# Kernel optimization log

Measured on AMD Instinct MI355X. Metric: run time of the kernel, lower is better.

Reference implementation:

```python
import jax, jax.numpy as jnp
import numpy as np
from jax import lax


def _conv(x, w):
    # x: [B,H,W,C], w: [kh,kw,Cin,Cout], stride 1, 'same' padding
    return lax.conv_general_dilated(x, w, window_strides=(1, 1), padding='SAME',
                                    dimension_numbers=('NHWC', 'HWIO', 'NHWC'))


def setup_inputs() -> dict:
    key = jax.random.key(0)
    ks = jax.random.split(key, 4)
    B, T, H, W, Cin, F = 16, 5, 256, 256, 3, 8
    return {
        'input_tensor': jax.random.normal(ks[0], (B, T, H, W, Cin), jnp.float32),
        'kernel': jax.random.normal(ks[1], (3, 3, Cin, 4 * F), jnp.float32) * 0.1,
        'recurrent_kernel': jax.random.normal(ks[2], (3, 3, F, 4 * F), jnp.float32) * 0.1,
        'bias': jnp.zeros((4 * F,), jnp.float32),
        'gamma': jnp.ones((F,), jnp.float32),
        'beta': jnp.zeros((F,), jnp.float32),
        'moving_mean': jnp.zeros((F,), jnp.float32),
        'moving_var': jnp.ones((F,), jnp.float32),
        'dense_w': jax.random.normal(ks[3], (F, 2), jnp.float32) * 0.1,
        'dense_b': jnp.zeros((2,), jnp.float32),
    }


def reference(input_tensor, kernel, recurrent_kernel, bias, gamma, beta,
              moving_mean, moving_var, dense_w, dense_b):
    B, T, H, W, Cin = input_tensor.shape
    F = recurrent_kernel.shape[2]
    xs = jnp.moveaxis(input_tensor, 1, 0)  # [T,B,H,W,Cin] time-major for scan
    h0 = jnp.zeros((B, H, W, F), input_tensor.dtype)

    def step(carry, x_t):
        h, c = carry
        # fused 4-gate pre-activations, Keras gate order: i, f, c(g), o
        z = _conv(x_t, kernel) + _conv(h, recurrent_kernel) + bias
        i, f, g, o = jnp.split(z, 4, axis=-1)
        i = jax.nn.sigmoid(i)
        f = jax.nn.sigmoid(f)
        g = jnp.tanh(g)
        o = jax.nn.sigmoid(o)
        c = f * c + i * g
        h = o * jnp.tanh(c)
        return (h, c), None

    (h, _), _ = lax.scan(step, (h0, h0), xs)  # return_sequences=False -> last h

    # BatchNormalization (inference, Keras eps=1e-3)
    eps = 1e-3
    x = (h - moving_mean) * lax.rsqrt(moving_var + eps) * gamma + beta
    # LeakyReLU, Keras default alpha=0.3
    x = jnp.where(x >= 0, x, 0.3 * x)
    # Dense(2) over channel dim
    return jnp.einsum('bhwf,fk->bhwk', x, dense_w) + dense_b
```

## Files before the change

kernel.cpp:

```cpp
#include <hip/hip_runtime.h>


#define BB  16
#define TT  5
#define HH  256
#define WW  256
#define CIN 3
#define FF  8
#define GG  32

#define TWO 32
#define THO 32
#define RW  40
#define RH  40
#define LWW 42
#define LHH 42
#define NR  10

#define LOG2E 1.44269504088896340736f

typedef _Float16 half8  __attribute__((ext_vector_type(8)));
typedef _Float16 half4  __attribute__((ext_vector_type(4)));
typedef float    floatx4 __attribute__((ext_vector_type(4)));

__device__ __forceinline__ float frcp(float x) { return __builtin_amdgcn_rcpf(x); }
__device__ __forceinline__ float sig2(float z)  { return frcp(1.0f + __builtin_amdgcn_exp2f(z)); }
__device__ __forceinline__ float tanh2(float z) { return 1.0f - 2.0f * frcp(1.0f + __builtin_amdgcn_exp2f(z)); }

#define MFMA(A, B, C) __builtin_amdgcn_mfma_f32_16x16x32_f16((A), (B), (C), 0, 0, 0)

__global__ void build_frags(const float* __restrict__ wk,
                            const float* __restrict__ wr,
                            _Float16* __restrict__ blob) {
    const int lane = threadIdx.x & 63;
    const int quad = lane >> 4, nlo = lane & 15;
    for (int chunk = 0; chunk < 5; ++chunk) {
        for (int nh = 0; nh < 2; ++nh) {
            const int n = nh * 16 + nlo;
            const float scale = (n >= 16 && n < 24) ? (2.0f * LOG2E) : (-LOG2E);
            const int frag = chunk * 2 + nh;
            _Float16* dhi = blob + ((size_t)frag * 64 + lane) * 8;
            _Float16* dlo = (chunk >= 2)
                ? blob + ((size_t)(10 + (chunk - 2) * 2 + nh) * 64 + lane) * 8
                : nullptr;
            for (int j = 0; j < 8; ++j) {
                const int k = quad * 8 + j;
                float w = 0.0f;
                if (chunk == 0) {
                    int tap = k >> 2, ci = k & 3;
                    if (ci < 3) w = wk[(tap * 3 + ci) * GG + n];
                } else if (chunk == 1) {
                    if (quad == 0 && j < 3) w = wk[(8 * 3 + j) * GG + n];
                } else {
                    int c = chunk - 2;
                    int tap = c * 4 + quad, ci = j;
                    if (tap < 9) w = wr[(tap * FF + ci) * GG + n];
                }
                w *= scale;
                _Float16 wh = (_Float16)w;
                dhi[j] = wh;
                if (dlo) dlo[j] = (_Float16)(w - (float)wh);
            }
        }
    }
}

__global__ __launch_bounds__(256, 2) void lstm_fused(
    const float* __restrict__ xg,
    const _Float16* __restrict__ blob,
    const float* __restrict__ bias,
    const float* __restrict__ gamma, const float* __restrict__ beta,
    const float* __restrict__ mean,  const float* __restrict__ var,
    const float* __restrict__ dw,    const float* __restrict__ db,
    float* __restrict__ out)
{
    __shared__ half8 hAs[LHH * LWW];
    __shared__ half8 hBs[LHH * LWW];
    __shared__ half4 xls[LHH * LWW];

    const int tid  = threadIdx.x;
    const int bx = blockIdx.x, by = blockIdx.y, b = blockIdx.z;
    const int lane = tid & 63, wave = tid >> 6;
    const int quad = lane >> 4, nlo = lane & 15;
    const bool lo8 = (nlo < 8);
    const int fc = nlo & 7;

    const int xt0 = 2 * quad, xt1 = xt0 + 1;
    const int xoff0 = (xt0 / 3) * LWW + (xt0 % 3);
    const int xoff1 = (xt1 / 3) * LWW + (xt1 % 3);
    const int xoff2 = 2 * LWW + 2;
    int hoff[3];
#pragma unroll
    for (int c = 0; c < 3; ++c) {
        int tap = c * 4 + quad;
        if (tap > 8) tap = 8;
        hoff[c] = (tap / 3) * LWW + (tap % 3);
    }

    half8 bfh[10], bfl[6];
#pragma unroll
    for (int i = 0; i < 10; ++i)
        bfh[i] = *(const half8*)(blob + ((size_t)i * 64 + lane) * 8);
#pragma unroll
    for (int i = 0; i < 6; ++i)
        bfl[i] = *(const half8*)(blob + ((size_t)(10 + i) * 64 + lane) * 8);

    const float bv0 = bias[nlo] * (-LOG2E);
    const float bv1 = bias[16 + nlo] * (lo8 ? 2.0f * LOG2E : -LOG2E);

    const float bn_s = gamma[fc] * rsqrtf(var[fc] + 1e-3f);
    const float bn_b = beta[fc] - mean[fc] * bn_s;
    const float dw0 = dw[fc * 2 + 0], dw1 = dw[fc * 2 + 1];
    const float db0 = db[0], db1 = db[1];

    const half8 hz = {(_Float16)0, (_Float16)0, (_Float16)0, (_Float16)0,
                      (_Float16)0, (_Float16)0, (_Float16)0, (_Float16)0};
    for (int l = tid; l < LHH * LWW; l += 256) { hAs[l] = hz; hBs[l] = hz; }

    float c0r[NR][3], c1r[NR][3];
#pragma unroll
    for (int r = 0; r < NR; ++r)
#pragma unroll
        for (int s = 0; s < 3; ++s) { c0r[r][s] = 0.f; c1r[r][s] = 0.f; }

    for (int t = 0; t < TT; ++t) {
        half8* hRd = (t & 1) ? hAs : hBs;
        half8* hWr = (t & 1) ? hBs : hAs;

        for (int l = tid; l < LHH * LWW; l += 256) {
            int rr = l / LWW, rc = l - rr * LWW;
            int iy = by * THO + rr - 5;
            int ix = bx * TWO + rc - 5;
            half4 vh = {(_Float16)0, (_Float16)0, (_Float16)0, (_Float16)0};
            if ((unsigned)iy < HH && (unsigned)ix < WW) {
                const float* p = xg + (((size_t)(b * TT + t) * HH + iy) * WW + ix) * CIN;
                vh.x = (_Float16)p[0]; vh.y = (_Float16)p[1]; vh.z = (_Float16)p[2];
            }
            xls[l] = vh;
        }
        __syncthreads();

#pragma unroll 1
        for (int r10 = 0; r10 < NR; ++r10) {
            const int row = wave * NR + r10;
            const int rowbase = row * LWW + nlo;

            half4 xp[3], xq[3], xs_[3];
            half8 ah[3][3];
#pragma unroll
            for (int s = 0; s < 3; ++s) {
                const int base = rowbase + s * 12;
                xp[s]  = xls[base + xoff0];
                xq[s]  = xls[base + xoff1];
                xs_[s] = xls[base + xoff2];
                if (t > 0) {
#pragma unroll
                    for (int c = 0; c < 3; ++c)
                        ah[s][c] = hRd[base + hoff[c]];
                }
            }

#pragma unroll
            for (int s = 0; s < 3; ++s) {
                const int gx0 = s * 12;

                half8 a_xA = (half8){xp[s].x, xp[s].y, xp[s].z, xp[s].w,
                                     xq[s].x, xq[s].y, xq[s].z, xq[s].w};
                half8 a_xB = (half8){xs_[s].x, xs_[s].y, xs_[s].z, xs_[s].w,
                                     xs_[s].x, xs_[s].y, xs_[s].z, xs_[s].w};

                floatx4 acc0 = {bv0, bv0, bv0, bv0};
                floatx4 acc1 = {bv1, bv1, bv1, bv1};
                acc0 = MFMA(a_xA, bfh[0], acc0);  acc1 = MFMA(a_xA, bfh[1], acc1);
                acc0 = MFMA(a_xB, bfh[2], acc0);  acc1 = MFMA(a_xB, bfh[3], acc1);
                if (t > 0) {
#pragma unroll
                    for (int c = 0; c < 3; ++c) {
                        acc0 = MFMA(ah[s][c], bfh[4 + c * 2], acc0);
                        acc1 = MFMA(ah[s][c], bfh[5 + c * 2], acc1);
                        acc0 = MFMA(ah[s][c], bfl[c * 2 + 0], acc0);
                        acc1 = MFMA(ah[s][c], bfl[c * 2 + 1], acc1);
                    }
                }

                float s0 = lo8 ? acc0[2] : acc0[0]; float r0 = __shfl_xor(s0, 8, 64);
                float s1 = lo8 ? acc0[3] : acc0[1]; float r1 = __shfl_xor(s1, 8, 64);
                float s2 = lo8 ? acc1[2] : acc1[0]; float r2 = __shfl_xor(s2, 8, 64);
                float s3 = lo8 ? acc1[3] : acc1[1]; float r3 = __shfl_xor(s3, 8, 64);

                const float zi0 = lo8 ? acc0[0] : r0, zi1 = lo8 ? acc0[1] : r1;
                const float zf0 = lo8 ? r0 : acc0[2], zf1 = lo8 ? r1 : acc0[3];
                const float zg0 = lo8 ? acc1[0] : r2, zg1 = lo8 ? acc1[1] : r3;
                const float zo0 = lo8 ? r2 : acc1[2], zo1 = lo8 ? r3 : acc1[3];

                const float ii0 = sig2(zi0), ff0 = sig2(zf0), gg0 = tanh2(zg0), oo0 = sig2(zo0);
                const float cn0 = ff0 * c0r[r10][s] + ii0 * gg0;
                const float hn0 = oo0 * tanh2(cn0 * (2.0f * LOG2E));
                const float ii1 = sig2(zi1), ff1 = sig2(zf1), gg1 = tanh2(zg1), oo1 = sig2(zo1);
                const float cn1 = ff1 * c1r[r10][s] + ii1 * gg1;
                const float hn1 = oo1 * tanh2(cn1 * (2.0f * LOG2E));
                c0r[r10][s] = cn0; c1r[r10][s] = cn1;

                const int m0 = quad * 4 + (lo8 ? 0 : 2);
                const int iy  = by * THO + row - 4;
                const int ix0 = bx * TWO + gx0 + m0 - 4;
                if (t < TT - 1) {
                    const bool iny = (unsigned)iy < HH;
                    const int idx = (row + 1) * LWW + (gx0 + m0 + 1);
                    _Float16* hp = (_Float16*)hWr;
                    hp[idx * 8 + fc] =
                        (iny && (unsigned)ix0 < WW) ? (_Float16)hn0 : (_Float16)0;
                    hp[(idx + 1) * 8 + fc] =
                        (iny && (unsigned)(ix0 + 1) < WW) ? (_Float16)hn1 : (_Float16)0;
                } else {
                    float y0 = bn_s * hn0 + bn_b; y0 = (y0 >= 0.f) ? y0 : 0.3f * y0;
                    float y1 = bn_s * hn1 + bn_b; y1 = (y1 >= 0.f) ? y1 : 0.3f * y1;
                    float p00 = y0 * dw0, p01 = y0 * dw1;
                    float p10 = y1 * dw0, p11 = y1 * dw1;
#pragma unroll
                    for (int m = 1; m <= 4; m <<= 1) {
                        p00 += __shfl_xor(p00, m, 64);
                        p01 += __shfl_xor(p01, m, 64);
                        p10 += __shfl_xor(p10, m, 64);
                        p11 += __shfl_xor(p11, m, 64);
                    }
                    const int j = nlo & 7;
                    if (j < 4) {
                        const int rc = gx0 + m0 + (j >> 1);
                        const int k  = j & 1;
                        if (rc >= 4 && rc < 36 && row >= 4 && row < 36) {
                            const int ox = bx * TWO + rc - 4;
                            const int oy = by * THO + row - 4;
                            float val = (j == 0 ? p00 : j == 1 ? p01 : j == 2 ? p10 : p11)
                                        + (k ? db1 : db0);
                            out[((size_t)(b * HH + oy) * WW + ox) * 2 + k] = val;
                        }
                    }
                }
            }
        }
        __syncthreads();
    }
}

extern "C" void kernel_launch(void* const* d_in, const int* in_sizes, int n_in,
                              void* d_out, int out_size, void* d_ws, size_t ws_size,
                              hipStream_t stream) {
    const float* x     = (const float*)d_in[0];
    const float* wk    = (const float*)d_in[1];
    const float* wr    = (const float*)d_in[2];
    const float* bias  = (const float*)d_in[3];
    const float* gamma = (const float*)d_in[4];
    const float* beta  = (const float*)d_in[5];
    const float* mean  = (const float*)d_in[6];
    const float* var   = (const float*)d_in[7];
    const float* dw    = (const float*)d_in[8];
    const float* db    = (const float*)d_in[9];
    float* out = (float*)d_out;

    _Float16* blob = (_Float16*)d_ws;

    build_frags<<<1, 64, 0, stream>>>(wk, wr, blob);

    dim3 grid(WW / TWO, HH / THO, BB);
    dim3 block(256);
    lstm_fused<<<grid, block, 0, stream>>>(
        x, blob, bias, gamma, beta, mean, var, dw, db, out);
}
```

Measured before the change: 304.3 us.

## Split time loop into three launches with global h/c state and smaller halos

Replaces the single fused kernel, which recomputed a 4-pixel halo per tile across all 5 timesteps, with three templated launches covering steps 0-1, 2-3 and 4. Between launches h and c are stored to global memory in fp16. This shrinks the halo to 2 pixels and the LDS tiles (34x22), cutting redundant halo compute and allowing more resident blocks. The cost is extra global traffic for the h/c state and launch overhead, and storing c in fp16 loses some precision.

```diff
diff --git a/kernel.cpp b/kernel.cpp
--- a/kernel.cpp
+++ b/kernel.cpp
@@ -9,13 +9,14 @@
 #define FF  8
 #define GG  32
 
-#define TWO 32
-#define THO 32
-#define RW  40
-#define RH  40
-#define LWW 42
-#define LHH 42
-#define NR  10
+#define TWO 28
+#define THO 16
+#define RW  32
+#define RH  20
+#define LWW 34
+#define LHH 22
+#define NRW 5
+#define GX  10
 
 #define LOG2E 1.44269504088896340736f
 
@@ -65,10 +66,15 @@
     }
 }
 
-__global__ __launch_bounds__(256, 2) void lstm_fused(
+template <int T0, int NS, bool FIRST, bool LAST>
+__global__ __launch_bounds__(256) void lstm_multi(
     const float* __restrict__ xg,
     const _Float16* __restrict__ blob,
     const float* __restrict__ bias,
+    const _Float16* __restrict__ hin,
+    _Float16* __restrict__ hout,
+    const _Float16* __restrict__ cin,
+    _Float16* __restrict__ cout,
     const float* __restrict__ gamma, const float* __restrict__ beta,
     const float* __restrict__ mean,  const float* __restrict__ var,
     const float* __restrict__ dw,    const float* __restrict__ db,
@@ -84,6 +90,7 @@
     const int quad = lane >> 4, nlo = lane & 15;
     const bool lo8 = (nlo < 8);
     const int fc = nlo & 7;
+    const int m0 = quad * 4 + (lo8 ? 0 : 2);
 
     const int xt0 = 2 * quad, xt1 = xt0 + 1;
     const int xoff0 = (xt0 / 3) * LWW + (xt0 % 3);
@@ -108,78 +115,109 @@
     const float bv0 = bias[nlo] * (-LOG2E);
     const float bv1 = bias[16 + nlo] * (lo8 ? 2.0f * LOG2E : -LOG2E);
 
-    const float bn_s = gamma[fc] * rsqrtf(var[fc] + 1e-3f);
-    const float bn_b = beta[fc] - mean[fc] * bn_s;
-    const float dw0 = dw[fc * 2 + 0], dw1 = dw[fc * 2 + 1];
-    const float db0 = db[0], db1 = db[1];
+    float bn_s = 0.f, bn_b = 0.f, dw0 = 0.f, dw1 = 0.f, db0 = 0.f, db1 = 0.f;
+    if (LAST) {
+        bn_s = gamma[fc] * rsqrtf(var[fc] + 1e-3f);
+        bn_b = beta[fc] - mean[fc] * bn_s;
+        dw0 = dw[fc * 2 + 0]; dw1 = dw[fc * 2 + 1];
+        db0 = db[0]; db1 = db[1];
+    }
 
     const half8 hz = {(_Float16)0, (_Float16)0, (_Float16)0, (_Float16)0,
                       (_Float16)0, (_Float16)0, (_Float16)0, (_Float16)0};
     for (int l = tid; l < LHH * LWW; l += 256) { hAs[l] = hz; hBs[l] = hz; }
 
-    float c0r[NR][3], c1r[NR][3];
-#pragma unroll
-    for (int r = 0; r < NR; ++r)
-#pragma unroll
-        for (int s = 0; s < 3; ++s) { c0r[r][s] = 0.f; c1r[r][s] = 0.f; }
-
-    for (int t = 0; t < TT; ++t) {
-        half8* hRd = (t & 1) ? hAs : hBs;
-        half8* hWr = (t & 1) ? hBs : hAs;
-
+    float c0r[NRW][2], c1r[NRW][2];
+#pragma unroll
+    for (int r = 0; r < NRW; ++r) { c0r[r][0] = c0r[r][1] = 0.f;
+                                    c1r[r][0] = c1r[r][1] = 0.f; }
+    if (!FIRST) {
+#pragma unroll
+        for (int r = 0; r < NRW; ++r) {
+#pragma unroll
+            for (int st = 0; st < 2; ++st) {
+                const int row = wave * NRW + r;
+                const int iy  = by * THO + row - 2;
+                const int ix0 = bx * TWO + st * 16 + m0 - 2;
+                if ((unsigned)iy < HH) {
+                    const size_t base = ((size_t)(b * HH + iy) * WW) * FF + fc;
+                    if ((unsigned)ix0 < WW)
+                        c0r[r][st] = (float)cin[base + (size_t)ix0 * FF];
+                    if ((unsigned)(ix0 + 1) < WW)
+                        c1r[r][st] = (float)cin[base + (size_t)(ix0 + 1) * FF];
+                }
+            }
+        }
         for (int l = tid; l < LHH * LWW; l += 256) {
             int rr = l / LWW, rc = l - rr * LWW;
-            int iy = by * THO + rr - 5;
-            int ix = bx * TWO + rc - 5;
+            int iy = by * THO + rr - 3, ix = bx * TWO + rc - 3;
+            half8 v = hz;
+            if ((unsigned)iy < HH && (unsigned)ix < WW)
+                v = *(const half8*)(hin + ((size_t)(b * HH + iy) * WW + ix) * FF);
+            hAs[l] = v;
+        }
+    }
+
+#pragma unroll
+    for (int s = 0; s < NS; ++s) {
+        __syncthreads();
+
+        for (int l = tid; l < LHH * LWW; l += 256) {
+            int rr = l / LWW, rc = l - rr * LWW;
+            int iy = by * THO + rr - 3, ix = bx * TWO + rc - 3;
             half4 vh = {(_Float16)0, (_Float16)0, (_Float16)0, (_Float16)0};
             if ((unsigned)iy < HH && (unsigned)ix < WW) {
-                const float* p = xg + (((size_t)(b * TT + t) * HH + iy) * WW + ix) * CIN;
+                const float* p = xg + (((size_t)(b * TT + T0 + s) * HH + iy) * WW + ix) * CIN;
                 vh.x = (_Float16)p[0]; vh.y = (_Float16)p[1]; vh.z = (_Float16)p[2];
             }
             xls[l] = vh;
         }
         __syncthreads();
 
-#pragma unroll 1
-        for (int r10 = 0; r10 < NR; ++r10) {
-            const int row = wave * NR + r10;
+        const bool hconv = (s > 0) || !FIRST;
+        half8* hRd = (s & 1) ? hBs : hAs;
+        half8* hWr = (s & 1) ? hAs : hBs;
+
+#pragma unroll
+        for (int r = 0; r < NRW; ++r) {
+            const int row = wave * NRW + r;
             const int rowbase = row * LWW + nlo;
 
-            half4 xp[3], xq[3], xs_[3];
-            half8 ah[3][3];
-#pragma unroll
-            for (int s = 0; s < 3; ++s) {
-                const int base = rowbase + s * 12;
-                xp[s]  = xls[base + xoff0];
-                xq[s]  = xls[base + xoff1];
-                xs_[s] = xls[base + xoff2];
-                if (t > 0) {
+            half4 xp[2], xq[2], xs_[2];
+            half8 ah[2][3];
+#pragma unroll
+            for (int st = 0; st < 2; ++st) {
+                const int base = rowbase + st * 16;
+                xp[st]  = xls[base + xoff0];
+                xq[st]  = xls[base + xoff1];
+                xs_[st] = xls[base + xoff2];
+                if (hconv) {
 #pragma unroll
                     for (int c = 0; c < 3; ++c)
-                        ah[s][c] = hRd[base + hoff[c]];
-                }
-            }
-
-#pragma unroll
-            for (int s = 0; s < 3; ++s) {
-                const int gx0 = s * 12;
-
-                half8 a_xA = (half8){xp[s].x, xp[s].y, xp[s].z, xp[s].w,
-                                     xq[s].x, xq[s].y, xq[s].z, xq[s].w};
-                half8 a_xB = (half8){xs_[s].x, xs_[s].y, xs_[s].z, xs_[s].w,
-                                     xs_[s].x, xs_[s].y, xs_[s].z, xs_[s].w};
+                        ah[st][c] = hRd[base + hoff[c]];
+                }
+            }
+
+#pragma unroll
+            for (int st = 0; st < 2; ++st) {
+                const int gx0 = st * 16;
+
+                half8 a_xA = (half8){xp[st].x, xp[st].y, xp[st].z, xp[st].w,
+                                     xq[st].x, xq[st].y, xq[st].z, xq[st].w};
+                half8 a_xB = (half8){xs_[st].x, xs_[st].y, xs_[st].z, xs_[st].w,
+                                     xs_[st].x, xs_[st].y, xs_[st].z, xs_[st].w};
 
                 floatx4 acc0 = {bv0, bv0, bv0, bv0};
                 floatx4 acc1 = {bv1, bv1, bv1, bv1};
                 acc0 = MFMA(a_xA, bfh[0], acc0);  acc1 = MFMA(a_xA, bfh[1], acc1);
                 acc0 = MFMA(a_xB, bfh[2], acc0);  acc1 = MFMA(a_xB, bfh[3], acc1);
-                if (t > 0) {
+                if (hconv) {
 #pragma unroll
                     for (int c = 0; c < 3; ++c) {
-                        acc0 = MFMA(ah[s][c], bfh[4 + c * 2], acc0);
-                        acc1 = MFMA(ah[s][c], bfh[5 + c * 2], acc1);
-                        acc0 = MFMA(ah[s][c], bfl[c * 2 + 0], acc0);
-                        acc1 = MFMA(ah[s][c], bfl[c * 2 + 1], acc1);
+                        acc0 = MFMA(ah[st][c], bfh[4 + c * 2], acc0);
+                        acc1 = MFMA(ah[st][c], bfh[5 + c * 2], acc1);
+                        acc0 = MFMA(ah[st][c], bfl[c * 2 + 0], acc0);
+                        acc1 = MFMA(ah[st][c], bfl[c * 2 + 1], acc1);
                     }
                 }
 
@@ -194,24 +232,38 @@
                 const float zo0 = lo8 ? r2 : acc1[2], zo1 = lo8 ? r3 : acc1[3];
 
                 const float ii0 = sig2(zi0), ff0 = sig2(zf0), gg0 = tanh2(zg0), oo0 = sig2(zo0);
-                const float cn0 = ff0 * c0r[r10][s] + ii0 * gg0;
+                const float cn0 = ff0 * c0r[r][st] + ii0 * gg0;
                 const float hn0 = oo0 * tanh2(cn0 * (2.0f * LOG2E));
                 const float ii1 = sig2(zi1), ff1 = sig2(zf1), gg1 = tanh2(zg1), oo1 = sig2(zo1);
-                const float cn1 = ff1 * c1r[r10][s] + ii1 * gg1;
+                const float cn1 = ff1 * c1r[r][st] + ii1 * gg1;
                 const float hn1 = oo1 * tanh2(cn1 * (2.0f * LOG2E));
-                c0r[r10][s] = cn0; c1r[r10][s] = cn1;
-
-                const int m0 = quad * 4 + (lo8 ? 0 : 2);
-                const int iy  = by * THO + row - 4;
-                const int ix0 = bx * TWO + gx0 + m0 - 4;
-                if (t < TT - 1) {
+                c0r[r][st] = cn0; c1r[r][st] = cn1;
+
+                const int iy  = by * THO + row - 2;
+                const int pc0 = gx0 + m0;
+                const int ix0 = bx * TWO + pc0 - 2;
+
+                if (s < NS - 1) {
                     const bool iny = (unsigned)iy < HH;
-                    const int idx = (row + 1) * LWW + (gx0 + m0 + 1);
+                    const int idx = (row + 1) * LWW + (pc0 + 1);
                     _Float16* hp = (_Float16*)hWr;
                     hp[idx * 8 + fc] =
                         (iny && (unsigned)ix0 < WW) ? (_Float16)hn0 : (_Float16)0;
                     hp[(idx + 1) * 8 + fc] =
                         (iny && (unsigned)(ix0 + 1) < WW) ? (_Float16)hn1 : (_Float16)0;
+                } else if (!LAST) {
+                    const bool trow = (row >= 2 && row < 2 + THO);
+                    const bool t0ok = trow && pc0 >= 2 && pc0 < 2 + TWO && (unsigned)ix0 < WW;
+                    const bool t1ok = trow && pc0 + 1 >= 2 && pc0 + 1 < 2 + TWO &&
+                                      (unsigned)(ix0 + 1) < WW;
+                    if (t0ok) {
+                        const size_t p = ((size_t)(b * HH + iy) * WW + ix0) * FF + fc;
+                        hout[p] = (_Float16)hn0; cout[p] = (_Float16)cn0;
+                    }
+                    if (t1ok) {
+                        const size_t p = ((size_t)(b * HH + iy) * WW + ix0 + 1) * FF + fc;
+                        hout[p] = (_Float16)hn1; cout[p] = (_Float16)cn1;
+                    }
                 } else {
                     float y0 = bn_s * hn0 + bn_b; y0 = (y0 >= 0.f) ? y0 : 0.3f * y0;
                     float y1 = bn_s * hn1 + bn_b; y1 = (y1 >= 0.f) ? y1 : 0.3f * y1;
@@ -226,11 +278,12 @@
                     }
                     const int j = nlo & 7;
                     if (j < 4) {
-                        const int rc = gx0 + m0 + (j >> 1);
+                        const int rc = pc0 + (j >> 1);
                         const int k  = j & 1;
-                        if (rc >= 4 && rc < 36 && row >= 4 && row < 36) {
-                            const int ox = bx * TWO + rc - 4;
-                            const int oy = by * THO + row - 4;
+                        const int ox = bx * TWO + rc - 2;
+                        if (rc >= 2 && rc < 2 + TWO && (unsigned)ox < WW &&
+                            row >= 2 && row < 2 + THO) {
+                            const int oy = by * THO + row - 2;
                             float val = (j == 0 ? p00 : j == 1 ? p01 : j == 2 ? p10 : p11)
                                         + (k ? db1 : db0);
                             out[((size_t)(b * HH + oy) * WW + ox) * 2 + k] = val;
@@ -239,7 +292,6 @@
                 }
             }
         }
-        __syncthreads();
     }
 }
 
@@ -258,12 +310,21 @@
     const float* db    = (const float*)d_in[9];
     float* out = (float*)d_out;
 
+    const size_t state = (size_t)BB * HH * WW * FF;
     _Float16* blob = (_Float16*)d_ws;
+    _Float16* hA = (_Float16*)((char*)d_ws + 32768);
+    _Float16* hB = hA + state;
+    _Float16* cA = hB + state;
+    _Float16* cB = cA + state;
 
     build_frags<<<1, 64, 0, stream>>>(wk, wr, blob);
 
-    dim3 grid(WW / TWO, HH / THO, BB);
+    dim3 grid(GX, HH / THO, BB);
     dim3 block(256);
-    lstm_fused<<<grid, block, 0, stream>>>(
-        x, blob, bias, gamma, beta, mean, var, dw, db, out);
+    lstm_multi<0, 2, true,  false><<<grid, block, 0, stream>>>(
+        x, blob, bias, hA, hA, cA, cA, gamma, beta, mean, var, dw, db, out);
+    lstm_multi<2, 2, false, false><<<grid, block, 0, stream>>>(
+        x, blob, bias, hA, hB, cA, cB, gamma, beta, mean, var, dw, db, out);
+    lstm_multi<4, 1, false, true ><<<grid, block, 0, stream>>>(
+        x, blob, bias, hB, hB, cB, cB, gamma, beta, mean, var, dw, db, out);
 }
```

Result: slower. 356.3 us (+17.1%).
